# Performance work log

Measured on AMD Instinct MI355X. Metric: run time of the kernel, lower is better.

## Reference

```python
import jax, jax.numpy as jnp
import numpy as np

N = 20000
E = 320000
IN_C, HID, OUT_C = 128, 64, 32
H12, H3 = 4, 1  # heads for conv1/conv2 and conv3
NEG_SLOPE = 0.2


def _glorot(key, shape):
    fan_in, fan_out = shape[0], shape[-1]
    lim = (6.0 / (fan_in + fan_out)) ** 0.5
    return jax.random.uniform(key, shape, jnp.float32, -lim, lim)


def setup_inputs() -> dict:
    key = jax.random.key(0)
    ks = jax.random.split(key, 16)
    x = jax.random.normal(ks[0], (N, IN_C), jnp.float32)
    edge_index = jax.random.randint(ks[1], (2, E), 0, N, jnp.int64)
    p = {
        'W1': _glorot(ks[2], (IN_C, H12 * HID)),
        'as1': _glorot(ks[3], (H12, HID)), 'ad1': _glorot(ks[4], (H12, HID)),
        'b1': jnp.zeros((HID,), jnp.float32),
        'W2': _glorot(ks[5], (HID, H12 * HID)),
        'as2': _glorot(ks[6], (H12, HID)), 'ad2': _glorot(ks[7], (H12, HID)),
        'b2': jnp.zeros((HID,), jnp.float32),
        'W3': _glorot(ks[8], (HID, H3 * OUT_C)),
        'as3': _glorot(ks[9], (H3, OUT_C)), 'ad3': _glorot(ks[10], (H3, OUT_C)),
        'b3': jnp.zeros((OUT_C,), jnp.float32),
        'Wm': _glorot(ks[11], (OUT_C, OUT_C)), 'bm': jnp.zeros((OUT_C,), jnp.float32),
        'Wv': _glorot(ks[12], (OUT_C, OUT_C)), 'bv': jnp.zeros((OUT_C,), jnp.float32),
    }
    return dict(x=x, edge_index=edge_index, **p)


def gat_layer(x, src, dst, W, a_src, a_dst, b, heads, out_c):
    # x: [N, in_c] -> h: [N, H, C]
    h = (x @ W).reshape(-1, heads, out_c)
    alpha_s = jnp.einsum('nhc,hc->nh', h, a_src)  # [N,H]
    alpha_d = jnp.einsum('nhc,hc->nh', h, a_dst)
    e = jax.nn.leaky_relu(alpha_s[src] + alpha_d[dst], NEG_SLOPE)  # [E',H]
    # segment softmax over incoming edges of each dst node
    m = jax.ops.segment_max(e, dst, num_segments=N)
    p = jnp.exp(e - m[dst])
    s = jax.ops.segment_sum(p, dst, num_segments=N)
    alpha = p / (s[dst] + 1e-16)  # [E',H]
    msg = h[src] * alpha[:, :, None]  # [E',H,C]
    out = jax.ops.segment_sum(msg, dst, num_segments=N)  # [N,H,C]
    return out.mean(axis=1) + b  # concat=False -> mean over heads


def reference(x, edge_index, W1, as1, ad1, b1, W2, as2, ad2, b2,
              W3, as3, ad3, b3, Wm, bm, Wv, bv):
    # PyG GATConv default: add self loops
    loop = jnp.arange(N, dtype=edge_index.dtype)
    src = jnp.concatenate([edge_index[0], loop])
    dst = jnp.concatenate([edge_index[1], loop])

    h = jax.nn.relu(gat_layer(x, src, dst, W1, as1, ad1, b1, H12, HID))
    h = jax.nn.relu(gat_layer(h, src, dst, W2, as2, ad2, b2, H12, HID))
    z = gat_layer(h, src, dst, W3, as3, ad3, b3, H3, OUT_C)

    z_mean = z @ Wm + bm
    z_var = jnp.clip(jnp.exp(z @ Wv + bv), 1e-8, 100.0)
    return (z_mean, z_var, z)
```

## Files before the change

### kernel.cpp

```cpp
#include <hip/hip_runtime.h>
#include <hip/hip_bf16.h>

typedef unsigned short ushortT;
typedef short short8 __attribute__((ext_vector_type(8)));
typedef unsigned short ushort8v __attribute__((ext_vector_type(8)));
typedef float float4v __attribute__((ext_vector_type(4)));

constexpr int Nn   = 20000;
constexpr int Ee   = 320000;
constexpr int EP   = Ee + Nn;
constexpr float NSL = 0.2f;
constexpr int CAP  = 128;

__device__ __forceinline__ float b2f(__hip_bfloat16 v) { return __bfloat162float(v); }
__device__ __forceinline__ float bits2f(unsigned short u) {
    __hip_bfloat16 b; *(unsigned short*)&b = u; return __bfloat162float(b);
}
__device__ __forceinline__ unsigned short f2bits(float v) {
    __hip_bfloat16 b = __float2bfloat16(v); return *(unsigned short*)&b;
}
__device__ __forceinline__ float ldf(const void* p, size_t i, int bf) {
    return bf ? __bfloat162float(((const __hip_bfloat16*)p)[i])
              : ((const float*)p)[i];
}
__device__ __forceinline__ void stf(void* p, size_t i, float v, int bf) {
    if (bf) ((__hip_bfloat16*)p)[i] = __float2bfloat16(v);
    else    ((float*)p)[i] = v;
}

__global__ void probe_k(const int* __restrict__ ei, const unsigned* __restrict__ xbits,
                        int* __restrict__ eflag, int* __restrict__ fflag) {
    __shared__ int bad, cnt;
    if (threadIdx.x == 0) { bad = 0; cnt = 0; }
    __syncthreads();
    for (int i = threadIdx.x; i < 1024; i += blockDim.x)
        if (ei[2 * i + 1] != 0) bad = 1;
    int c = 0;
    for (int i = threadIdx.x; i < 512; i += blockDim.x) {
        unsigned e = (xbits[i] >> 7) & 0xFFu;
        if (e >= 110u && e <= 135u) ++c;
    }
    atomicAdd(&cnt, c);
    __syncthreads();
    if (threadIdx.x == 0) {
        *eflag = bad ? 0 : 1;
        *fflag = (cnt > 384) ? 1 : 0;
    }
}

__device__ __forceinline__ void load_edge(const int* __restrict__ ei, int sh, int e,
                                          int& si, int& di) {
    if (e < Ee) {
        si = ei[(size_t)e << sh];
        di = ei[(size_t)(Ee + e) << sh];
    } else {
        si = di = e - Ee;
    }
}

__global__ void prep_k(const void* __restrict__ W1, const void* __restrict__ W2,
                       ushortT* __restrict__ WT1, ushortT* __restrict__ WT2,
                       const int* __restrict__ fflag) {
    const int bf = *fflag;
    int idx = blockIdx.x * 256 + threadIdx.x;
    if (idx < 256 * 128) {
        int j = idx >> 7, k = idx & 127;
        WT1[idx] = f2bits(ldf(W1, (size_t)k * 256 + j, bf));
    } else {
        int i2 = idx - 256 * 128;
        if (i2 < 256 * 64) {
            int j = i2 >> 6, k = i2 & 63;
            WT2[i2] = f2bits(ldf(W2, (size_t)k * 256 + j, bf));
        }
    }
}

__global__ void scatter_k(const int* __restrict__ ei, const int* __restrict__ eflag,
                          int* __restrict__ cnt, int* __restrict__ csr) {
    int e = blockIdx.x * 256 + threadIdx.x;
    if (e >= EP) return;
    int sh = *eflag, si, di;
    load_edge(ei, sh, e, si, di);
    int pos = atomicAdd(cnt + di, 1);
    if (pos < CAP) csr[di * CAP + pos] = si;
}

template <int XMODE, int INC>
__global__ __launch_bounds__(256) void gemm_mfma(const void* __restrict__ xg,
                                                 const ushortT* __restrict__ WT,
                                                 ushortT* __restrict__ h,
                                                 const void* __restrict__ avs,
                                                 const void* __restrict__ avd,
                                                 float* __restrict__ as_, float* __restrict__ ad_,
                                                 const int* __restrict__ fflag) {
    constexpr int SW = INC + 8, SX = INC + 8, CPR = INC / 8;
    const int bf  = *fflag;
    const int xbf = (XMODE == 0) ? bf : 1;
    __shared__ ushortT wt_s[128 * SW];
    __shared__ ushortT xs[64 * SX];
    const int base = blockIdx.x * 64;
    const int jh   = blockIdx.y;
    const ushortT* WTg = WT + (size_t)jh * 128 * INC;
    for (int ch = threadIdx.x; ch < 128 * CPR; ch += 256) {
        int j = ch / CPR, kc = (ch - j * CPR) * 8;
        *(short8*)(wt_s + j * SW + kc) = *(const short8*)(WTg + j * INC + kc);
    }
    for (int ch = threadIdx.x; ch < 64 * CPR; ch += 256) {
        int nl = ch / CPR, kc = (ch - nl * CPR) * 8;
        int node = base + nl;
        short8 v = {0, 0, 0, 0, 0, 0, 0, 0};
        if (node < Nn) {
            if (xbf) {
                v = *(const short8*)((const ushortT*)xg + (size_t)node * INC + kc);
            } else {
                const float* xf = (const float*)xg + (size_t)node * INC + kc;
#pragma unroll
                for (int i = 0; i < 8; ++i) v[i] = (short)f2bits(xf[i]);
            }
        }
        *(short8*)(xs + nl * SX + kc) = v;
    }
    __syncthreads();
    const int lane = threadIdx.x & 63, w = threadIdx.x >> 6;
    const int ln = lane & 15, quad = lane >> 4;
    float4v acc[8];
#pragma unroll
    for (int T = 0; T < 8; ++T) acc[T] = (float4v){0.f, 0.f, 0.f, 0.f};
#pragma unroll
    for (int ks = 0; ks < INC / 32; ++ks) {
        const int kb = ks * 32 + quad * 8;
        const short8 b = *(const short8*)(xs + (w * 16 + ln) * SX + kb);
#pragma unroll
        for (int T = 0; T < 8; ++T) {
            const short8 a = *(const short8*)(wt_s + (T * 16 + ln) * SW + kb);
            acc[T] = __builtin_amdgcn_mfma_f32_16x16x32_bf16(a, b, acc[T], 0, 0, 0);
        }
    }
    const int node = base + w * 16 + ln;
    const bool live = (node < Nn);
    ushortT* hn = h + (size_t)node * 256;
    float pas0 = 0, pas1 = 0, pad0 = 0, pad1 = 0;
#pragma unroll
    for (int T = 0; T < 8; ++T) {
        const int jb = jh * 128 + T * 16 + quad * 4;
#pragma unroll
        for (int r = 0; r < 4; ++r) {
            const int j = jb + r;
            const float v = acc[T][r];
            if (live) hn[(j & 63) * 4 + (j >> 6)] = f2bits(v);
            const float was = ldf(avs, j, bf), wad = ldf(avd, j, bf);
            if (T < 4) { pas0 = fmaf(v, was, pas0); pad0 = fmaf(v, wad, pad0); }
            else       { pas1 = fmaf(v, was, pas1); pad1 = fmaf(v, wad, pad1); }
        }
    }
#pragma unroll
    for (int off = 16; off < 64; off <<= 1) {
        pas0 += __shfl_xor(pas0, off, 64);
        pas1 += __shfl_xor(pas1, off, 64);
        pad0 += __shfl_xor(pad0, off, 64);
        pad1 += __shfl_xor(pad1, off, 64);
    }
    if (lane < 16 && live) {
        as_[node * 4 + jh * 2]     = pas0;
        as_[node * 4 + jh * 2 + 1] = pas1;
        ad_[node * 4 + jh * 2]     = pad0;
        ad_[node * 4 + jh * 2 + 1] = pad1;
    }
}

__global__ __launch_bounds__(256) void gemm_small(const float* __restrict__ x,
                                                  const void* __restrict__ W,
                                                  __hip_bfloat16* __restrict__ h,
                                                  const void* __restrict__ avs,
                                                  const void* __restrict__ avd,
                                                  float* __restrict__ as_, float* __restrict__ ad_,
                                                  const int* __restrict__ fflag, int N) {
    constexpr int INC = 64, R = 32, PAD = R + 4;
    const int bf = *fflag;
    __shared__ float xsh[INC * PAD];
    int base = blockIdx.x * R;
    for (int i = threadIdx.x; i < R * INC; i += 256) {
        int rr = i / INC, kk = i - rr * INC;
        int nn = base + rr;
        xsh[kk * PAD + rr] = (nn < N) ? x[(size_t)nn * INC + kk] : 0.0f;
    }
    __syncthreads();
    const int jc = threadIdx.x & 31;
    const int g  = threadIdx.x >> 5;
    float acc[4] = {};
    if (bf) {
        const __hip_bfloat16* Wb = (const __hip_bfloat16*)W;
#pragma unroll 4
        for (int k = 0; k < INC; ++k) {
            float4 xv = *(const float4*)(xsh + k * PAD + g * 4);
            float w = b2f(Wb[k * 32 + jc]);
            acc[0] = fmaf(xv.x, w, acc[0]);
            acc[1] = fmaf(xv.y, w, acc[1]);
            acc[2] = fmaf(xv.z, w, acc[2]);
            acc[3] = fmaf(xv.w, w, acc[3]);
        }
    } else {
        const float* Wf = (const float*)W;
#pragma unroll 4
        for (int k = 0; k < INC; ++k) {
            float4 xv = *(const float4*)(xsh + k * PAD + g * 4);
            float w = Wf[k * 32 + jc];
            acc[0] = fmaf(xv.x, w, acc[0]);
            acc[1] = fmaf(xv.y, w, acc[1]);
            acc[2] = fmaf(xv.z, w, acc[2]);
            acc[3] = fmaf(xv.w, w, acc[3]);
        }
    }
    float avsr = ldf(avs, jc, bf), avdr = ldf(avd, jc, bf);
#pragma unroll
    for (int m = 0; m < 4; ++m) {
        int n = base + g * 4 + m;
        if (n >= N) continue;
        h[(size_t)n * 32 + jc] = __float2bfloat16(acc[m]);
        float t1 = acc[m] * avsr;
        float t2 = acc[m] * avdr;
#pragma unroll
        for (int off = 16; off > 0; off >>= 1) {
            t1 += __shfl_down(t1, off, 32);
            t2 += __shfl_down(t2, off, 32);
        }
        if (jc == 0) { as_[n] = t1; ad_[n] = t2; }
    }
}

__device__ __forceinline__ void agg_pair(const float* __restrict__ lal_row,
                                         const int* __restrict__ lof_row,
                                         int idx, bool valid,
                                         const ushortT* __restrict__ h, int cl, float* a) {
    float4 ev = valid ? *(const float4*)(lal_row + idx * 4) : make_float4(0.f, 0.f, 0.f, 0.f);
    int off = valid ? lof_row[idx] : 0;
    ushort8v hv = *(const ushort8v*)(h + off + cl * 8);
    a[0] = fmaf(ev.x, bits2f(hv[0]), a[0]);
    a[1] = fmaf(ev.y, bits2f(hv[1]), a[1]);
    a[2] = fmaf(ev.z, bits2f(hv[2]), a[2]);
    a[3] = fmaf(ev.w, bits2f(hv[3]), a[3]);
    a[4] = fmaf(ev.x, bits2f(hv[4]), a[4]);
    a[5] = fmaf(ev.y, bits2f(hv[5]), a[5]);
    a[6] = fmaf(ev.z, bits2f(hv[6]), a[6]);
    a[7] = fmaf(ev.w, bits2f(hv[7]), a[7]);
}

template <bool RELU>
__global__ __launch_bounds__(256) void aggr4_k(const int* __restrict__ cnt,
                                               const int* __restrict__ csr,
                                               const float* __restrict__ as_,
                                               const float* __restrict__ ad_,
                                               const unsigned short* __restrict__ h,
                                               const void* __restrict__ bias,
                                               const int* __restrict__ fflag,
                                               float* __restrict__ outF,
                                               ushortT* __restrict__ outB, int N) {
    __shared__ float lal[4][CAP][4];
    __shared__ int   lof[4][CAP];
    const int lane = threadIdx.x & 63, seg = threadIdx.x >> 6;
    int d = blockIdx.x * 4 + seg;
    if (d >= N) return;
    const int deg = min(cnt[d], CAP);
    const int base = d * CAP;
    const float4 adv = *(const float4*)(ad_ + d * 4);
    float s0 = 0, s1 = 0, s2 = 0, s3 = 0;
    for (int i = lane; i < deg; i += 64) {
        int src = csr[base + i];
        float4 av = *(const float4*)(as_ + src * 4);
        float v0 = av.x + adv.x; v0 = v0 > 0.f ? v0 : NSL * v0; float e0 = __expf(v0);
        float v1 = av.y + adv.y; v1 = v1 > 0.f ? v1 : NSL * v1; float e1 = __expf(v1);
        float v2 = av.z + adv.z; v2 = v2 > 0.f ? v2 : NSL * v2; float e2 = __expf(v2);
        float v3 = av.w + adv.w; v3 = v3 > 0.f ? v3 : NSL * v3; float e3 = __expf(v3);
        s0 += e0; s1 += e1; s2 += e2; s3 += e3;
        *(float4*)(&lal[seg][i][0]) = make_float4(e0, e1, e2, e3);
        lof[seg][i] = src * 256;
    }
#pragma unroll
    for (int off = 1; off < 64; off <<= 1) {
        s0 += __shfl_xor(s0, off, 64);
        s1 += __shfl_xor(s1, off, 64);
        s2 += __shfl_xor(s2, off, 64);
        s3 += __shfl_xor(s3, off, 64);
    }
    const float i0 = 0.25f / (s0 + 1e-16f), i1 = 0.25f / (s1 + 1e-16f);
    const float i2 = 0.25f / (s2 + 1e-16f), i3 = 0.25f / (s3 + 1e-16f);
    const int hl = lane >> 5, cl = lane & 31;
    const float* lal_s = &lal[seg][0][0];
    const int*   lof_s = &lof[seg][0];
    float a[8] = {0, 0, 0, 0, 0, 0, 0, 0};
    int e = 0;
    for (; e + 8 <= deg; e += 8) {
        agg_pair(lal_s, lof_s, e + hl,     true, h, cl, a);
        agg_pair(lal_s, lof_s, e + 2 + hl, true, h, cl, a);
        agg_pair(lal_s, lof_s, e + 4 + hl, true, h, cl, a);
        agg_pair(lal_s, lof_s, e + 6 + hl, true, h, cl, a);
    }
    for (; e < deg; e += 2)
        agg_pair(lal_s, lof_s, e + hl, (e + hl) < deg, h, cl, a);
#pragma unroll
    for (int i = 0; i < 8; ++i) a[i] += __shfl_xor(a[i], 32, 64);
    if (hl == 0) {
        const int bf = *fflag;
        float r0 = i0 * a[0] + i1 * a[1] + i2 * a[2] + i3 * a[3] + ldf(bias, 2 * cl, bf);
        float r1 = i0 * a[4] + i1 * a[5] + i2 * a[6] + i3 * a[7] + ldf(bias, 2 * cl + 1, bf);
        if (RELU) { r0 = fmaxf(r0, 0.f); r1 = fmaxf(r1, 0.f); }
        if (outF) *(float2*)(outF + (size_t)d * 64 + 2 * cl) = make_float2(r0, r1);
        if (outB) {
            ushort2 p; p.x = f2bits(r0); p.y = f2bits(r1);
            *(ushort2*)(outB + (size_t)d * 64 + 2 * cl) = p;
        }
    }
}

__global__ __launch_bounds__(256) void aggr1f_k(const int* __restrict__ cnt,
                                                const int* __restrict__ csr,
                                                const float* __restrict__ as_,
                                                const float* __restrict__ ad_,
                                                const __hip_bfloat16* __restrict__ h,
                                                const void* __restrict__ b3,
                                                const void* __restrict__ Wm,
                                                const void* __restrict__ bm,
                                                const void* __restrict__ Wv,
                                                const void* __restrict__ bv,
                                                const int* __restrict__ fflag,
                                                void* __restrict__ out, int N) {
    __shared__ float wm_s[1024], wv_s[1024];
    __shared__ float lal[8][CAP];
    __shared__ int   lof[8][CAP];
    const int bf = *fflag;
    for (int i = threadIdx.x; i < 1024; i += 256) {
        wm_s[i] = ldf(Wm, i, bf);
        wv_s[i] = ldf(Wv, i, bf);
    }
    __syncthreads();
    const int c = threadIdx.x & 31, seg = threadIdx.x >> 5;
    const int d = blockIdx.x * 8 + seg;
    if (d >= N) return;
    const int deg = min(cnt[d], CAP);
    const int base = d * CAP;
    const float advd = ad_[d];
    float s = 0;
    for (int i = c; i < deg; i += 32) {
        int src = csr[base + i];
        float v = as_[src] + advd;
        v = v > 0.f ? v : NSL * v;
        float ev = __expf(v);
        s += ev;
        lal[seg][i] = ev;
        lof[seg][i] = src * 32;
    }
#pragma unroll
    for (int off = 1; off < 32; off <<= 1) s += __shfl_xor(s, off, 32);
    const float inv = 1.0f / (s + 1e-16f);
    float acc = 0.0f;
    int e = 0;
    for (; e + 4 <= deg; e += 4) {
        float ev0 = lal[seg][e], ev1 = lal[seg][e + 1];
        float ev2 = lal[seg][e + 2], ev3 = lal[seg][e + 3];
        int o0 = lof[seg][e], o1 = lof[seg][e + 1];
        int o2 = lof[seg][e + 2], o3 = lof[seg][e + 3];
        float h0 = b2f(h[o0 + c]), h1 = b2f(h[o1 + c]);
        float h2 = b2f(h[o2 + c]), h3 = b2f(h[o3 + c]);
        acc = fmaf(ev0, h0, acc);
        acc = fmaf(ev1, h1, acc);
        acc = fmaf(ev2, h2, acc);
        acc = fmaf(ev3, h3, acc);
    }
    for (; e < deg; ++e) acc = fmaf(lal[seg][e], b2f(h[lof[seg][e] + c]), acc);
    const float z = inv * acc + ldf(b3, c, bf);
    stf(out, (size_t)2 * N * 32 + (size_t)d * 32 + c, z, bf);
    float sm = ldf(bm, c, bf), sv = ldf(bv, c, bf);
#pragma unroll 8
    for (int k = 0; k < 32; ++k) {
        float zk = __shfl(z, k, 32);
        sm = fmaf(zk, wm_s[k * 32 + c], sm);
        sv = fmaf(zk, wv_s[k * 32 + c], sv);
    }
    float var = __expf(sv);
    var = fminf(fmaxf(var, 1e-8f), 100.0f);
    stf(out, (size_t)d * 32 + c, sm, bf);
    stf(out, (size_t)N * 32 + (size_t)d * 32 + c, var, bf);
}

extern "C" void kernel_launch(void* const* d_in, const int* in_sizes, int n_in,
                              void* d_out, int out_size, void* d_ws, size_t ws_size,
                              hipStream_t stream) {
    const void* x   = d_in[0];
    const int*  ei  = (const int*)d_in[1];
    const void* W1  = d_in[2];
    const void* as1 = d_in[3];
    const void* ad1 = d_in[4];
    const void* b1  = d_in[5];
    const void* W2  = d_in[6];
    const void* as2 = d_in[7];
    const void* ad2 = d_in[8];
    const void* b2  = d_in[9];
    const void* W3  = d_in[10];
    const void* as3 = d_in[11];
    const void* ad3 = d_in[12];
    const void* b3  = d_in[13];
    const void* Wm  = d_in[14];
    const void* bm  = d_in[15];
    const void* Wv  = d_in[16];
    const void* bv  = d_in[17];

    float* ws = (float*)d_ws;
    ushortT* h    = (ushortT*)ws;
    ushortT* x1b  = (ushortT*)(ws + 2560000);
    float*  x2    = ws + 3200000;
    float*  as_   = ws + 4480000;
    float*  ad_   = ws + 4560000;
    ushortT* WT1  = (ushortT*)(ws + 4640000);
    ushortT* WT2  = (ushortT*)(ws + 4656384);
    int*    cnt   = (int*)(ws + 4664576);
    int*    csr   = (int*)(ws + 4684576);
    int*    eflag = (int*)(ws + 7244576);
    int*    fflag = (int*)(ws + 7244577);

    probe_k<<<1, 256, 0, stream>>>(ei, (const unsigned*)x, eflag, fflag);
    hipMemsetAsync(cnt, 0, (size_t)Nn * 4, stream);
    prep_k<<<192, 256, 0, stream>>>(W1, W2, WT1, WT2, fflag);
    scatter_k<<<(EP + 255) / 256, 256, 0, stream>>>(ei, eflag, cnt, csr);

    dim3 gg(313, 2);
    gemm_mfma<0, 128><<<gg, 256, 0, stream>>>(x, WT1, h, as1, ad1, as_, ad_, fflag);
    aggr4_k<true><<<5000, 256, 0, stream>>>(cnt, csr, as_, ad_, h, b1, fflag,
                                            nullptr, x1b, Nn);

    gemm_mfma<1, 64><<<gg, 256, 0, stream>>>(x1b, WT2, h, as2, ad2, as_, ad_, fflag);
    aggr4_k<true><<<5000, 256, 0, stream>>>(cnt, csr, as_, ad_, h, b2, fflag,
                                            x2, nullptr, Nn);

    gemm_small<<<625, 256, 0, stream>>>(x2, W3, (__hip_bfloat16*)h, as3, ad3, as_, ad_, fflag, Nn);
    aggr1f_k<<<2500, 256, 0, stream>>>(cnt, csr, as_, ad_, (const __hip_bfloat16*)h,
                                       b3, Wm, bm, Wv, bv, fflag, d_out, Nn);
}
```

Before: 242.2 us.

## Keep CSR sources in registers, fuse cnt memset into probe, defer sum reductions

Folds the cnt zeroing into the probe kernel (now 79 blocks), which removes one memset launch. In the 4-head aggregation kernel, each lane keeps up to two CSR source indices in registers and broadcasts them with shuffles, replacing the shared-memory offset array. In both aggregation kernels the softmax-sum wave reduction moves after the gather loop so it can overlap with the memory loads. The cost is extra shuffles per gathered edge and a hard assumption that degree is at most 128 (CAP).

```diff
diff --git a/kernel.cpp b/kernel.cpp
--- a/kernel.cpp
+++ b/kernel.cpp
@@ -29,22 +29,26 @@
 }
 
 __global__ void probe_k(const int* __restrict__ ei, const unsigned* __restrict__ xbits,
-                        int* __restrict__ eflag, int* __restrict__ fflag) {
-    __shared__ int bad, cnt;
-    if (threadIdx.x == 0) { bad = 0; cnt = 0; }
+                        int* __restrict__ eflag, int* __restrict__ fflag,
+                        int* __restrict__ cnt) {
+    int gi = blockIdx.x * 256 + threadIdx.x;
+    if (gi < Nn) cnt[gi] = 0;
+    if (blockIdx.x != 0) return;
+    __shared__ int bad, c_s;
+    if (threadIdx.x == 0) { bad = 0; c_s = 0; }
     __syncthreads();
-    for (int i = threadIdx.x; i < 1024; i += blockDim.x)
+    for (int i = threadIdx.x; i < 1024; i += 256)
         if (ei[2 * i + 1] != 0) bad = 1;
     int c = 0;
-    for (int i = threadIdx.x; i < 512; i += blockDim.x) {
+    for (int i = threadIdx.x; i < 512; i += 256) {
         unsigned e = (xbits[i] >> 7) & 0xFFu;
         if (e >= 110u && e <= 135u) ++c;
     }
-    atomicAdd(&cnt, c);
+    atomicAdd(&c_s, c);
     __syncthreads();
     if (threadIdx.x == 0) {
         *eflag = bad ? 0 : 1;
-        *fflag = (cnt > 384) ? 1 : 0;
+        *fflag = (c_s > 384) ? 1 : 0;
     }
 }
 
@@ -228,12 +232,14 @@
     }
 }
 
-__device__ __forceinline__ void agg_pair(const float* __restrict__ lal_row,
-                                         const int* __restrict__ lof_row,
-                                         int idx, bool valid,
-                                         const ushortT* __restrict__ h, int cl, float* a) {
+__device__ __forceinline__ void agg_pair2(int idx, bool valid, int src0, int src1,
+                                          const float* __restrict__ lal_row,
+                                          const ushortT* __restrict__ h, int cl, float* a) {
+    int sa = __shfl(src0, idx & 63, 64);
+    int sb = __shfl(src1, idx & 63, 64);
+    int src = (idx < 64) ? sa : sb;
+    int off = valid ? src * 256 : 0;
     float4 ev = valid ? *(const float4*)(lal_row + idx * 4) : make_float4(0.f, 0.f, 0.f, 0.f);
-    int off = valid ? lof_row[idx] : 0;
     ushort8v hv = *(const ushort8v*)(h + off + cl * 8);
     a[0] = fmaf(ev.x, bits2f(hv[0]), a[0]);
     a[1] = fmaf(ev.y, bits2f(hv[1]), a[1]);
@@ -256,25 +262,45 @@
                                                float* __restrict__ outF,
                                                ushortT* __restrict__ outB, int N) {
     __shared__ float lal[4][CAP][4];
-    __shared__ int   lof[4][CAP];
     const int lane = threadIdx.x & 63, seg = threadIdx.x >> 6;
     int d = blockIdx.x * 4 + seg;
     if (d >= N) return;
     const int deg = min(cnt[d], CAP);
     const int base = d * CAP;
     const float4 adv = *(const float4*)(ad_ + d * 4);
+    const int src0 = (lane < deg) ? csr[base + lane] : 0;
+    const int src1 = (64 + lane < deg) ? csr[base + 64 + lane] : 0;
     float s0 = 0, s1 = 0, s2 = 0, s3 = 0;
-    for (int i = lane; i < deg; i += 64) {
-        int src = csr[base + i];
-        float4 av = *(const float4*)(as_ + src * 4);
+    if (lane < deg) {
+        float4 av = *(const float4*)(as_ + src0 * 4);
         float v0 = av.x + adv.x; v0 = v0 > 0.f ? v0 : NSL * v0; float e0 = __expf(v0);
         float v1 = av.y + adv.y; v1 = v1 > 0.f ? v1 : NSL * v1; float e1 = __expf(v1);
         float v2 = av.z + adv.z; v2 = v2 > 0.f ? v2 : NSL * v2; float e2 = __expf(v2);
         float v3 = av.w + adv.w; v3 = v3 > 0.f ? v3 : NSL * v3; float e3 = __expf(v3);
         s0 += e0; s1 += e1; s2 += e2; s3 += e3;
-        *(float4*)(&lal[seg][i][0]) = make_float4(e0, e1, e2, e3);
-        lof[seg][i] = src * 256;
-    }
+        *(float4*)(&lal[seg][lane][0]) = make_float4(e0, e1, e2, e3);
+    }
+    if (64 + lane < deg) {
+        float4 av = *(const float4*)(as_ + src1 * 4);
+        float v0 = av.x + adv.x; v0 = v0 > 0.f ? v0 : NSL * v0; float e0 = __expf(v0);
+        float v1 = av.y + adv.y; v1 = v1 > 0.f ? v1 : NSL * v1; float e1 = __expf(v1);
+        float v2 = av.z + adv.z; v2 = v2 > 0.f ? v2 : NSL * v2; float e2 = __expf(v2);
+        float v3 = av.w + adv.w; v3 = v3 > 0.f ? v3 : NSL * v3; float e3 = __expf(v3);
+        s0 += e0; s1 += e1; s2 += e2; s3 += e3;
+        *(float4*)(&lal[seg][64 + lane][0]) = make_float4(e0, e1, e2, e3);
+    }
+    const int hl = lane >> 5, cl = lane & 31;
+    const float* lal_s = &lal[seg][0][0];
+    float a[8] = {0, 0, 0, 0, 0, 0, 0, 0};
+    int e = 0;
+    for (; e + 8 <= deg; e += 8) {
+        agg_pair2(e + hl,     true, src0, src1, lal_s, h, cl, a);
+        agg_pair2(e + 2 + hl, true, src0, src1, lal_s, h, cl, a);
+        agg_pair2(e + 4 + hl, true, src0, src1, lal_s, h, cl, a);
+        agg_pair2(e + 6 + hl, true, src0, src1, lal_s, h, cl, a);
+    }
+    for (; e < deg; e += 2)
+        agg_pair2(e + hl, (e + hl) < deg, src0, src1, lal_s, h, cl, a);
 #pragma unroll
     for (int off = 1; off < 64; off <<= 1) {
         s0 += __shfl_xor(s0, off, 64);
@@ -284,19 +310,6 @@
     }
     const float i0 = 0.25f / (s0 + 1e-16f), i1 = 0.25f / (s1 + 1e-16f);
     const float i2 = 0.25f / (s2 + 1e-16f), i3 = 0.25f / (s3 + 1e-16f);
-    const int hl = lane >> 5, cl = lane & 31;
-    const float* lal_s = &lal[seg][0][0];
-    const int*   lof_s = &lof[seg][0];
-    float a[8] = {0, 0, 0, 0, 0, 0, 0, 0};
-    int e = 0;
-    for (; e + 8 <= deg; e += 8) {
-        agg_pair(lal_s, lof_s, e + hl,     true, h, cl, a);
-        agg_pair(lal_s, lof_s, e + 2 + hl, true, h, cl, a);
-        agg_pair(lal_s, lof_s, e + 4 + hl, true, h, cl, a);
-        agg_pair(lal_s, lof_s, e + 6 + hl, true, h, cl, a);
-    }
-    for (; e < deg; e += 2)
-        agg_pair(lal_s, lof_s, e + hl, (e + hl) < deg, h, cl, a);
 #pragma unroll
     for (int i = 0; i < 8; ++i) a[i] += __shfl_xor(a[i], 32, 64);
     if (hl == 0) {
@@ -349,9 +362,6 @@
         lal[seg][i] = ev;
         lof[seg][i] = src * 32;
     }
-#pragma unroll
-    for (int off = 1; off < 32; off <<= 1) s += __shfl_xor(s, off, 32);
-    const float inv = 1.0f / (s + 1e-16f);
     float acc = 0.0f;
     int e = 0;
     for (; e + 4 <= deg; e += 4) {
@@ -367,6 +377,9 @@
         acc = fmaf(ev3, h3, acc);
     }
     for (; e < deg; ++e) acc = fmaf(lal[seg][e], b2f(h[lof[seg][e] + c]), acc);
+#pragma unroll
+    for (int off = 1; off < 32; off <<= 1) s += __shfl_xor(s, off, 32);
+    const float inv = 1.0f / (s + 1e-16f);
     const float z = inv * acc + ldf(b3, c, bf);
     stf(out, (size_t)2 * N * 32 + (size_t)d * 32 + c, z, bf);
     float sm = ldf(bm, c, bf), sv = ldf(bv, c, bf);
@@ -417,8 +430,7 @@
     int*    eflag = (int*)(ws + 7244576);
     int*    fflag = (int*)(ws + 7244577);
 
-    probe_k<<<1, 256, 0, stream>>>(ei, (const unsigned*)x, eflag, fflag);
-    hipMemsetAsync(cnt, 0, (size_t)Nn * 4, stream);
+    probe_k<<<79, 256, 0, stream>>>(ei, (const unsigned*)x, eflag, fflag, cnt);
     prep_k<<<192, 256, 0, stream>>>(W1, W2, WT1, WT2, fflag);
     scatter_k<<<(EP + 255) / 256, 256, 0, stream>>>(ei, eflag, cnt, csr);
 
```

Result: faster. 237.0 us (-2.1%).
